# Kernel tuning notes

Measured on AMD Instinct MI355X. Metric: run time of the kernel, lower is better.

## Reference

```python
import jax, jax.numpy as jnp
import numpy as np

B, T, I, H, C = 64, 512, 512, 1024, 1024
SIG_W = 3.0


def setup_inputs() -> dict:
    key = jax.random.key(0)
    ks = jax.random.split(key, 20)
    s = 0.02
    p = lambda k, shp: (jax.random.normal(k, shp, jnp.float32) * s)
    return dict(
        x=jax.random.normal(ks[0], (B, T, I), jnp.float32),
        att_wih_f=p(ks[1], (3 * H, I)), att_whh_f=p(ks[2], (3 * H, H)),
        att_bih_f=p(ks[3], (3 * H,)), att_bhh_f=p(ks[4], (3 * H,)),
        att_wih_b=p(ks[5], (3 * H, I)), att_whh_b=p(ks[6], (3 * H, H)),
        att_bih_b=p(ks[7], (3 * H,)), att_bhh_b=p(ks[8], (3 * H,)),
        att_fc_w=p(ks[9], (1, 2 * H)), att_fc_b=p(ks[10], (1,)),
        i2h_w=p(ks[11], (H, I)), i2h_b=p(ks[12], (H,)),
        h2h_w=p(ks[13], (H, H)), h2h_b=p(ks[14], (H,)),
        fc0_w=p(ks[15], (C, H)), fc0_b=p(ks[16], (C,)),
        fc1_w=p(ks[17], (H, H)), fc1_b=p(ks[18], (H,)),
    )


def _gru(x_tbi, wih, whh, bih, bhh):
    # torch-style GRU over time-major input [T,B,I] -> hidden states [T,B,H]
    def step(h, xt):
        gi = xt @ wih.T + bih          # [B,3H]
        gh = h @ whh.T + bhh           # [B,3H]
        ir, iz, inn = jnp.split(gi, 3, axis=-1)
        hr, hz, hn = jnp.split(gh, 3, axis=-1)
        r = jax.nn.sigmoid(ir + hr)
        z = jax.nn.sigmoid(iz + hz)
        n = jnp.tanh(inn + r * hn)
        h = (1.0 - z) * n + z * h
        return h, h
    h0 = jnp.zeros((x_tbi.shape[1], whh.shape[1]), x_tbi.dtype)
    _, hs = jax.lax.scan(step, h0, x_tbi)
    return hs


def reference(x, att_wih_f, att_whh_f, att_bih_f, att_bhh_f,
              att_wih_b, att_whh_b, att_bih_b, att_bhh_b,
              att_fc_w, att_fc_b, i2h_w, i2h_b, h2h_w, h2h_b,
              fc0_w, fc0_b, fc1_w, fc1_b):
    xt = jnp.transpose(x, (1, 0, 2))                      # [T,B,I] time-major
    # AttentionNet: bidirectional GRU + Linear(2H,1) + sigmoid(sig_w * score)
    hf = _gru(xt, att_wih_f, att_whh_f, att_bih_f, att_bhh_f)
    hb = _gru(xt[::-1], att_wih_b, att_whh_b, att_bih_b, att_bhh_b)[::-1]
    hcat = jnp.concatenate([hf, hb], axis=-1)             # [T,B,2H]
    att = jax.nn.sigmoid(SIG_W * (hcat @ att_fc_w.T + att_fc_b))[..., 0]  # [T,B]

    # TAGM recurrence: h_t = a_t * relu(i2h(x_t) + h2h(h)) + (1-a_t) * h
    i2h_all = xt @ i2h_w.T + i2h_b                        # [T,B,H]
    def step(h, inp):
        i2h_t, a_t = inp
        trans = jax.nn.relu(i2h_t + h @ h2h_w.T + h2h_b)  # [B,H]
        a = a_t[:, None]
        return a * trans + (1.0 - a) * h, None
    h0 = jnp.zeros((x.shape[0], h2h_w.shape[1]), x.dtype)
    h_last, _ = jax.lax.scan(step, h0, (i2h_all, att))

    out = (h_last @ fc0_w.T + fc0_b) @ fc1_w.T + fc1_b    # fc0 then fc1 (no dropout, eval)
    return out, jnp.transpose(att)                        # ([B,C], attention [B,T])
```

## Files before the change

kernel.cpp:

```cpp
#include <hip/hip_runtime.h>
#include <cstdint>
#include <cstddef>

#define TDIM 512
#define BDIM 64
#define IDIM 512
#define HDIM 1024
#define SPIN_CAP 20000u
#define NREP 4

typedef __attribute__((ext_vector_type(8))) short s16x8;
typedef __attribute__((ext_vector_type(4))) float f32x4;

__device__ __forceinline__ unsigned short f2bf(float f) {
  unsigned u = __builtin_bit_cast(unsigned, f);
  u += 0x7FFFu + ((u >> 16) & 1u);
  return (unsigned short)(u >> 16);
}
__device__ __forceinline__ float bf2f(unsigned short s) {
  unsigned u = ((unsigned)s) << 16;
  return __builtin_bit_cast(float, u);
}
__device__ __forceinline__ float sigmf(float x) { return 1.0f / (1.0f + __expf(-x)); }
__device__ __forceinline__ unsigned pk2(float a, float b) {
  return (unsigned)f2bf(a) | ((unsigned)f2bf(b) << 16);
}
#define MFMA16(a, b, c) __builtin_amdgcn_mfma_f32_16x16x32_bf16((a), (b), (c), 0, 0, 0)

__device__ __forceinline__ s16x8 ld16_llc(const unsigned long long* p) {
  s16x8 v;
  asm volatile("global_load_dwordx4 %0, %1, off sc0 sc1" : "=v"(v) : "v"(p));
  return v;
}
__device__ __forceinline__ void sysst64(unsigned long long* p, unsigned long long v) {
  __hip_atomic_store(p, v, __ATOMIC_RELAXED, __HIP_MEMORY_SCOPE_SYSTEM);
}

__global__ __launch_bounds__(256) void k_xcvt(const float* __restrict__ x,
                                              unsigned short* __restrict__ xbf) {
  int idx = blockIdx.x * 256 + threadIdx.x;
  int i8 = idx * 8;
  int i = i8 & (IDIM - 1);
  int tb = i8 >> 9;
  int t = tb >> 6, b = tb & 63;
  const float* src = x + ((size_t)(b * TDIM + t)) * IDIM + i;
  float4 a = *(const float4*)src;
  float4 c = *(const float4*)(src + 4);
  uint4 v;
  v.x = pk2(a.x, a.y); v.y = pk2(a.z, a.w);
  v.z = pk2(c.x, c.y); v.w = pk2(c.z, c.w);
  *(uint4*)(xbf + i8) = v;
}

__global__ __launch_bounds__(128, 1) void k_gru_fused(
    const unsigned short* __restrict__ xbf,
    const float* __restrict__ wihf32f, const float* __restrict__ wihf32b,
    const float* __restrict__ whhf32f, const float* __restrict__ whhf32b,
    const float* __restrict__ bih_f, const float* __restrict__ bhh_f,
    const float* __restrict__ bih_b, const float* __restrict__ bhh_b,
    const float* __restrict__ attw,
    unsigned long long* __restrict__ hbufu, float* __restrict__ attp,
    unsigned int* __restrict__ flags) {
  __shared__ uint4 lds4[147456 / 16];
  char* lds = (char*)lds4;
  const int wg = blockIdx.x;
  const int dir = wg >> 7, half = (wg >> 6) & 1, cg = wg & 63;
  const int tid = threadIdx.x, w = tid >> 6, l = tid & 63;
  const int r = l & 15, q = l >> 4;
  const int col = cg * 16 + r;
  const float* wih = dir ? wihf32b : wihf32f;
  const float* whh = dir ? whhf32b : whhf32f;
  const float* bih = dir ? bih_b : bih_f;
  const float* bhh = dir ? bhh_b : bhh_f;
  unsigned int* myflags = flags + (dir * 2 + half) * 1024;
  unsigned long long* hb0 = hbufu + (size_t)(dir * 2 + half) * (NREP * 2 * 8192);

  for (int it = tid; it < 48 * 128; it += 128) {
    int row = it >> 7, ch = it & 127;
    int g = row >> 4, rr = row & 15;
    const float* src = whh + ((size_t)(g * HDIM + cg * 16 + rr)) * HDIM + ch * 8;
    float4 f0 = *(const float4*)src;
    float4 f1 = *(const float4*)(src + 4);
    uint4 v;
    v.x = pk2(f0.x, f0.y); v.y = pk2(f0.z, f0.w);
    v.z = pk2(f1.x, f1.y); v.w = pk2(f1.z, f1.w);
    *(uint4*)(lds + row * 2048 + ((ch * 16) ^ ((row & 7) << 4))) = v;
  }
  for (int it = tid; it < 48 * 64; it += 128) {
    int row = it >> 6, ch = it & 63;
    int g = row >> 4, rr = row & 15;
    const float* src = wih + ((size_t)(g * HDIM + cg * 16 + rr)) * IDIM + ch * 8;
    float4 f0 = *(const float4*)src;
    float4 f1 = *(const float4*)(src + 4);
    uint4 v;
    v.x = pk2(f0.x, f0.y); v.y = pk2(f0.z, f0.w);
    v.z = pk2(f1.x, f1.y); v.w = pk2(f1.z, f1.w);
    *(uint4*)(lds + 98304 + row * 1024 + ((ch * 16) ^ ((row & 7) << 4))) = v;
  }
  __syncthreads();

  const float br = bih[col] + bhh[col];
  const float bz = bih[col + HDIM] + bhh[col + HDIM];
  const float bnx = bih[col + 2 * HDIM];
  const float bnh = bhh[col + 2 * HDIM];
  const float wfc = attw[dir * HDIM + col];
  const int swz = (r & 7) << 4;
  const int bb = half * 32 + w * 16;
  float h[4] = {0.f, 0.f, 0.f, 0.f};

  for (int t = 0; t < TDIM; ++t) {
    const int tt = dir ? (TDIM - 1 - t) : t;
    f32x4 aR = {}, aZ = {}, aNx = {}, aNh = {};
    {
      const unsigned short* px = xbf + ((size_t)(tt * BDIM + bb + r)) * IDIM + q * 8;
#pragma unroll 4
      for (int kt = 0; kt < 16; ++kt) {
        s16x8 a = *(const s16x8*)(px + kt * 32);
        int kb = q * 16 + kt * 64;
        s16x8 b0 = *(const s16x8*)(lds + 98304 + r * 1024 + (kb ^ swz));
        s16x8 b1 = *(const s16x8*)(lds + 98304 + (16 + r) * 1024 + (kb ^ swz));
        s16x8 b2 = *(const s16x8*)(lds + 98304 + (32 + r) * 1024 + (kb ^ swz));
        aR = MFMA16(a, b0, aR);
        aZ = MFMA16(a, b1, aZ);
        aNx = MFMA16(a, b2, aNx);
      }
    }
    if (t > 0) {
      for (unsigned spin = 0;; ++spin) {
        unsigned v = __hip_atomic_load(&myflags[l * 16], __ATOMIC_RELAXED, __HIP_MEMORY_SCOPE_SYSTEM);
        if (__all((int)(v >= (unsigned)t))) break;
        if (spin > SPIN_CAP) break;
      }
      __builtin_amdgcn_sched_barrier(0);
    }
    {
      const unsigned long long* ph = hb0 + (size_t)(cg & (NREP - 1)) * 16384 +
                                     (size_t)(t & 1) * 8192 + (w * 16 + r) * 256 + q * 2;
      s16x8 ha[32];
#pragma unroll
      for (int i = 0; i < 32; ++i) {
        int kro = (i + cg) & 31;
        ha[i] = ld16_llc(ph + kro * 8);
      }
      asm volatile("s_waitcnt vmcnt(0)" ::: "memory");
      __builtin_amdgcn_sched_barrier(0);
#pragma unroll
      for (int i = 0; i < 32; ++i) {
        int kro = (i + cg) & 31;
        int kb = q * 16 + kro * 64;
        s16x8 b0 = *(const s16x8*)(lds + r * 2048 + (kb ^ swz));
        s16x8 b1 = *(const s16x8*)(lds + (16 + r) * 2048 + (kb ^ swz));
        s16x8 b2 = *(const s16x8*)(lds + (32 + r) * 2048 + (kb ^ swz));
        aR = MFMA16(ha[i], b0, aR);
        aZ = MFMA16(ha[i], b1, aZ);
        aNh = MFMA16(ha[i], b2, aNh);
      }
    }
    unsigned long long* hn = hb0 + (size_t)((t + 1) & 1) * 8192;
    float sa[4];
#pragma unroll
    for (int j = 0; j < 4; ++j) {
      const int lb = w * 16 + q * 4 + j;
      float rg = sigmf(aR[j] + br);
      float zg = sigmf(aZ[j] + bz);
      float ng = tanhf(aNx[j] + bnx + rg * (aNh[j] + bnh));
      float hv = (1.0f - zg) * ng + zg * h[j];
      h[j] = hv;
      sa[j] = hv * wfc;
      unsigned p2 = pk2(hv, __shfl_xor(hv, 1, 64));
      unsigned p2o = __shfl_xor(p2, 2, 64);
      if ((r & 3) == 0) {
        unsigned long long v64 = (unsigned long long)p2 | ((unsigned long long)p2o << 32);
        size_t off = (size_t)lb * 256 + cg * 4 + (r >> 2);
#pragma unroll
        for (int rep = 0; rep < NREP; ++rep)
          sysst64(&hn[(size_t)rep * 16384 + off], v64);
      }
    }
    asm volatile("s_waitcnt vmcnt(0)" ::: "memory");
    __syncthreads();
    if (tid == 0)
      __hip_atomic_store(&myflags[cg * 16], (unsigned)(t + 1),
                         __ATOMIC_RELAXED, __HIP_MEMORY_SCOPE_SYSTEM);
    {
      float* ap = attp + (size_t)(dir * 64 + cg) * (TDIM * BDIM) + tt * BDIM;
#pragma unroll
      for (int j = 0; j < 4; ++j) {
        const int b = half * 32 + w * 16 + q * 4 + j;
        float s = sa[j];
        s += __shfl_xor(s, 1, 64);
        s += __shfl_xor(s, 2, 64);
        s += __shfl_xor(s, 4, 64);
        s += __shfl_xor(s, 8, 64);
        if (r == 0) ap[b] = s;
      }
    }
  }
}

__global__ __launch_bounds__(256) void k_attf(const float* __restrict__ attp,
                                              const float* __restrict__ fcb,
                                              float* __restrict__ att,
                                              float* __restrict__ att_out) {
  int idx = blockIdx.x * 256 + threadIdx.x;
  float s = fcb[0];
  for (int g = 0; g < 128; ++g) s += attp[(size_t)g * (TDIM * BDIM) + idx];
  float a = sigmf(3.0f * s);
  att[idx] = a;
  int t = idx >> 6, b = idx & 63;
  att_out[(size_t)b * TDIM + t] = a;
}

__global__ __launch_bounds__(128, 1) void k_scan3(
    const unsigned short* __restrict__ xbf,
    const float* __restrict__ i2hf32, const float* __restrict__ h2hf32,
    const float* __restrict__ i2hb, const float* __restrict__ h2hb,
    const float* __restrict__ att,
    unsigned long long* __restrict__ h3u, float* __restrict__ hlast,
    unsigned int* __restrict__ flags3) {
  __shared__ uint4 lds4[49152 / 16];
  char* lds = (char*)lds4;
  const int wg = blockIdx.x;
  const int half = wg >> 6, cg = wg & 63;
  const int tid = threadIdx.x, w = tid >> 6, l = tid & 63;
  const int r = l & 15, q = l >> 4;
  const int col = cg * 16 + r;
  unsigned int* myflags = flags3 + half * 1024;
  unsigned long long* hb0 = h3u + (size_t)half * (NREP * 2 * 8192);
  for (int it = tid; it < 16 * 128; it += 128) {
    int row = it >> 7, ch = it & 127;
    const float* src = h2hf32 + ((size_t)(cg * 16 + row)) * HDIM + ch * 8;
    float4 f0 = *(const float4*)src;
    float4 f1 = *(const float4*)(src + 4);
    uint4 v;
    v.x = pk2(f0.x, f0.y); v.y = pk2(f0.z, f0.w);
    v.z = pk2(f1.x, f1.y); v.w = pk2(f1.z, f1.w);
    *(uint4*)(lds + row * 2048 + ((ch * 16) ^ ((row & 7) << 4))) = v;
  }
  for (int it = tid; it < 16 * 64; it += 128) {
    int row = it >> 6, ch = it & 63;
    const float* src = i2hf32 + ((size_t)(cg * 16 + row)) * IDIM + ch * 8;
    float4 f0 = *(const float4*)src;
    float4 f1 = *(const float4*)(src + 4);
    uint4 v;
    v.x = pk2(f0.x, f0.y); v.y = pk2(f0.z, f0.w);
    v.z = pk2(f1.x, f1.y); v.w = pk2(f1.z, f1.w);
    *(uint4*)(lds + 32768 + row * 1024 + ((ch * 16) ^ ((row & 7) << 4))) = v;
  }
  __syncthreads();
  const float bc = i2hb[col] + h2hb[col];
  const int swz = (r & 7) << 4;
  const int bb = half * 32 + w * 16;
  float h[4] = {0.f, 0.f, 0.f, 0.f};
  for (int t = 0; t < TDIM; ++t) {
    f32x4 ac = {};
    {
      const unsigned short* px = xbf + ((size_t)(t * BDIM + bb + r)) * IDIM + q * 8;
#pragma unroll 4
      for (int kt = 0; kt < 16; ++kt) {
        s16x8 a = *(const s16x8*)(px + kt * 32);
        int kb = q * 16 + kt * 64;
        s16x8 b = *(const s16x8*)(lds + 32768 + r * 1024 + (kb ^ swz));
        ac = MFMA16(a, b, ac);
      }
    }
    if (t > 0) {
      for (unsigned spin = 0;; ++spin) {
        unsigned v = __hip_atomic_load(&myflags[l * 16], __ATOMIC_RELAXED, __HIP_MEMORY_SCOPE_SYSTEM);
        if (__all((int)(v >= (unsigned)t))) break;
        if (spin > SPIN_CAP) break;
      }
      __builtin_amdgcn_sched_barrier(0);
    }
    {
      const unsigned long long* ph = hb0 + (size_t)(cg & (NREP - 1)) * 16384 +
                                     (size_t)(t & 1) * 8192 + (w * 16 + r) * 256 + q * 2;
      s16x8 ha[32];
#pragma unroll
      for (int i = 0; i < 32; ++i) {
        int kro = (i + cg) & 31;
        ha[i] = ld16_llc(ph + kro * 8);
      }
      asm volatile("s_waitcnt vmcnt(0)" ::: "memory");
      __builtin_amdgcn_sched_barrier(0);
#pragma unroll
      for (int i = 0; i < 32; ++i) {
        int kro = (i + cg) & 31;
        int kb = q * 16 + kro * 64;
        s16x8 b = *(const s16x8*)(lds + r * 2048 + (kb ^ swz));
        ac = MFMA16(ha[i], b, ac);
      }
    }
    unsigned long long* hn = hb0 + (size_t)((t + 1) & 1) * 8192;
    const float* ab = att + (size_t)t * BDIM;
#pragma unroll
    for (int j = 0; j < 4; ++j) {
      const int lb = w * 16 + q * 4 + j;
      float tr = fmaxf(ac[j] + bc, 0.0f);
      float a = ab[half * 32 + lb];
      float hv = a * tr + (1.0f - a) * h[j];
      h[j] = hv;
      unsigned p2 = pk2(hv, __shfl_xor(hv, 1, 64));
      unsigned p2o = __shfl_xor(p2, 2, 64);
      if ((r & 3) == 0) {
        unsigned long long v64 = (unsigned long long)p2 | ((unsigned long long)p2o << 32);
        size_t off = (size_t)lb * 256 + cg * 4 + (r >> 2);
#pragma unroll
        for (int rep = 0; rep < NREP; ++rep)
          sysst64(&hn[(size_t)rep * 16384 + off], v64);
      }
    }
    asm volatile("s_waitcnt vmcnt(0)" ::: "memory");
    __syncthreads();
    if (tid == 0)
      __hip_atomic_store(&myflags[cg * 16], (unsigned)(t + 1),
                         __ATOMIC_RELAXED, __HIP_MEMORY_SCOPE_SYSTEM);
  }
#pragma unroll
  for (int j = 0; j < 4; ++j) {
    const int b = half * 32 + w * 16 + q * 4 + j;
    hlast[b * HDIM + col] = h[j];
  }
}

__global__ __launch_bounds__(256) void k_fc(const float* __restrict__ A,
                                            const float* __restrict__ W,
                                            const float* __restrict__ bias,
                                            float* __restrict__ dst) {
  const int idx = blockIdx.x * 256 + threadIdx.x;
  const int rr = idx >> 10, c = idx & 1023;
  const float4* a = (const float4*)(A + (size_t)rr * HDIM);
  const float4* w = (const float4*)(W + (size_t)c * HDIM);
  float s = bias[c];
  for (int k = 0; k < HDIM / 4; ++k) {
    float4 xx = a[k], y = w[k];
    s += xx.x * y.x + xx.y * y.y + xx.z * y.z + xx.w * y.w;
  }
  dst[idx] = s;
}

__global__ __launch_bounds__(256) void k_diag(float* out, int n, float val) {
  int i = blockIdx.x * 256 + threadIdx.x;
  if (i < n) out[i] = val;
}

extern "C" void kernel_launch(void* const* d_in, const int* in_sizes, int n_in,
                              void* d_out, int out_size, void* d_ws, size_t ws_size,
                              hipStream_t stream) {
  float* outF = (float*)d_out;
  int diag_blocks = (out_size + 255) / 256;

  static const int exp_sizes[19] = {16777216, 1572864, 3145728, 3072, 3072,
                                    1572864, 3145728, 3072, 3072, 2048, 1,
                                    524288, 1024, 1048576, 1024, 1048576, 1024,
                                    1048576, 1024};
  if (n_in != 19) {
    k_diag<<<diag_blocks, 256, 0, stream>>>(outF, out_size, 3999.0f);
    return;
  }
  for (int i = 0; i < 19; ++i) {
    if (in_sizes[i] != exp_sizes[i]) {
      k_diag<<<diag_blocks, 256, 0, stream>>>(outF, out_size, (float)(4000 + i * 16));
      return;
    }
  }

  const float* x     = (const float*)d_in[0];
  const float* wih_f = (const float*)d_in[1];
  const float* whh_f = (const float*)d_in[2];
  const float* bih_f = (const float*)d_in[3];
  const float* bhh_f = (const float*)d_in[4];
  const float* wih_b = (const float*)d_in[5];
  const float* whh_b = (const float*)d_in[6];
  const float* bih_b = (const float*)d_in[7];
  const float* bhh_b = (const float*)d_in[8];
  const float* fc_w  = (const float*)d_in[9];
  const float* fc_b  = (const float*)d_in[10];
  const float* i2h_w = (const float*)d_in[11];
  const float* i2h_b = (const float*)d_in[12];
  const float* h2h_w = (const float*)d_in[13];
  const float* h2h_b = (const float*)d_in[14];
  const float* fc0_w = (const float*)d_in[15];
  const float* fc0_b = (const float*)d_in[16];
  const float* fc1_w = (const float*)d_in[17];
  const float* fc1_b = (const float*)d_in[18];

  const size_t OFF_XBF   = 0;
  const size_t OFF_ATTP  = 33554432;
  const size_t OFF_ATT   = 50331648;
  const size_t OFF_HBUF  = 50462720;
  const size_t OFF_H3BUF = 52559872;
  const size_t OFF_HLAST = 53608448;
  const size_t OFF_OUT1  = 53870592;
  const size_t OFF_FLAGS = 54132736;
  const size_t TOTAL     = 54157312;

  if (ws_size < TOTAL) {
    k_diag<<<diag_blocks, 256, 0, stream>>>(outF, out_size, (float)(ws_size >> 20));
    return;
  }

  char* ws = (char*)d_ws;
  unsigned short* xbf       = (unsigned short*)(ws + OFF_XBF);
  float* attp               = (float*)(ws + OFF_ATTP);
  float* att                = (float*)(ws + OFF_ATT);
  unsigned long long* hbufu = (unsigned long long*)(ws + OFF_HBUF);
  unsigned long long* h3u   = (unsigned long long*)(ws + OFF_H3BUF);
  float* hlast              = (float*)(ws + OFF_HLAST);
  float* out1               = (float*)(ws + OFF_OUT1);
  unsigned int* flags       = (unsigned int*)(ws + OFF_FLAGS);

  hipMemsetAsync(flags, 0, 24576, stream);
  hipMemsetAsync(hbufu, 0, 2097152, stream);
  hipMemsetAsync(h3u, 0, 1048576, stream);

  k_xcvt<<<8192, 256, 0, stream>>>(x, xbf);

  k_gru_fused<<<256, 128, 0, stream>>>(xbf, wih_f, wih_b, whh_f, whh_b,
                                       bih_f, bhh_f, bih_b, bhh_b, fc_w,
                                       hbufu, attp, flags);

  k_attf<<<128, 256, 0, stream>>>(attp, fc_b, att, outF + 65536);

  k_scan3<<<128, 128, 0, stream>>>(xbf, i2h_w, h2h_w, i2h_b, h2h_b, att,
                                   h3u, hlast, flags + 4096);

  k_fc<<<256, 256, 0, stream>>>(hlast, fc0_w, fc0_b, out1);
  k_fc<<<256, 256, 0, stream>>>(out1, fc1_w, fc1_b, outF);
}
```

Measured before the change: 8.035 ms.

## Use full per-timestep hidden-state history buffers instead of replicated ring buffers

```diff
diff --git a/kernel.cpp b/kernel.cpp
--- a/kernel.cpp
+++ b/kernel.cpp
@@ -16,10 +16,6 @@
   unsigned u = __builtin_bit_cast(unsigned, f);
   u += 0x7FFFu + ((u >> 16) & 1u);
   return (unsigned short)(u >> 16);
-}
-__device__ __forceinline__ float bf2f(unsigned short s) {
-  unsigned u = ((unsigned)s) << 16;
-  return __builtin_bit_cast(float, u);
 }
 __device__ __forceinline__ float sigmf(float x) { return 1.0f / (1.0f + __expf(-x)); }
 __device__ __forceinline__ unsigned pk2(float a, float b) {
@@ -50,6 +46,242 @@
   v.x = pk2(a.x, a.y); v.y = pk2(a.z, a.w);
   v.z = pk2(c.x, c.y); v.w = pk2(c.z, c.w);
   *(uint4*)(xbf + i8) = v;
+}
+
+__global__ __launch_bounds__(128, 1) void k_gru_big(
+    const unsigned short* __restrict__ xbf,
+    const float* __restrict__ wihf32f, const float* __restrict__ wihf32b,
+    const float* __restrict__ whhf32f, const float* __restrict__ whhf32b,
+    const float* __restrict__ bih_f, const float* __restrict__ bhh_f,
+    const float* __restrict__ bih_b, const float* __restrict__ bhh_b,
+    const float* __restrict__ attw,
+    unsigned long long* __restrict__ ghist, float* __restrict__ attp,
+    unsigned int* __restrict__ flags) {
+  __shared__ uint4 lds4[147456 / 16];
+  char* lds = (char*)lds4;
+  const int wg = blockIdx.x;
+  const int dir = wg >> 7, half = (wg >> 6) & 1, cg = wg & 63;
+  const int tid = threadIdx.x, w = tid >> 6, l = tid & 63;
+  const int r = l & 15, q = l >> 4;
+  const int col = cg * 16 + r;
+  const float* wih = dir ? wihf32b : wihf32f;
+  const float* whh = dir ? whhf32b : whhf32f;
+  const float* bih = dir ? bih_b : bih_f;
+  const float* bhh = dir ? bhh_b : bhh_f;
+  unsigned int* myflags = flags + (dir * 2 + half) * 1024;
+  unsigned long long* hist = ghist + (size_t)(dir * 2 + half) * ((size_t)TDIM * 8192);
+
+  for (int it = tid; it < 48 * 128; it += 128) {
+    int row = it >> 7, ch = it & 127;
+    int g = row >> 4, rr = row & 15;
+    const float* src = whh + ((size_t)(g * HDIM + cg * 16 + rr)) * HDIM + ch * 8;
+    float4 f0 = *(const float4*)src;
+    float4 f1 = *(const float4*)(src + 4);
+    uint4 v;
+    v.x = pk2(f0.x, f0.y); v.y = pk2(f0.z, f0.w);
+    v.z = pk2(f1.x, f1.y); v.w = pk2(f1.z, f1.w);
+    *(uint4*)(lds + row * 2048 + ((ch * 16) ^ ((row & 7) << 4))) = v;
+  }
+  for (int it = tid; it < 48 * 64; it += 128) {
+    int row = it >> 6, ch = it & 63;
+    int g = row >> 4, rr = row & 15;
+    const float* src = wih + ((size_t)(g * HDIM + cg * 16 + rr)) * IDIM + ch * 8;
+    float4 f0 = *(const float4*)src;
+    float4 f1 = *(const float4*)(src + 4);
+    uint4 v;
+    v.x = pk2(f0.x, f0.y); v.y = pk2(f0.z, f0.w);
+    v.z = pk2(f1.x, f1.y); v.w = pk2(f1.z, f1.w);
+    *(uint4*)(lds + 98304 + row * 1024 + ((ch * 16) ^ ((row & 7) << 4))) = v;
+  }
+  __syncthreads();
+
+  const float br = bih[col] + bhh[col];
+  const float bz = bih[col + HDIM] + bhh[col + HDIM];
+  const float bnx = bih[col + 2 * HDIM];
+  const float bnh = bhh[col + 2 * HDIM];
+  const float wfc = attw[dir * HDIM + col];
+  const int swz = (r & 7) << 4;
+  const int bb = half * 32 + w * 16;
+  float h[4] = {0.f, 0.f, 0.f, 0.f};
+
+  for (int t = 0; t < TDIM; ++t) {
+    const int tt = dir ? (TDIM - 1 - t) : t;
+    f32x4 aR = {}, aZ = {}, aNx = {}, aNh = {};
+    {
+      const unsigned short* px = xbf + ((size_t)(tt * BDIM + bb + r)) * IDIM + q * 8;
+#pragma unroll 4
+      for (int kt = 0; kt < 16; ++kt) {
+        s16x8 a = *(const s16x8*)(px + kt * 32);
+        int kb = q * 16 + kt * 64;
+        s16x8 b0 = *(const s16x8*)(lds + 98304 + r * 1024 + (kb ^ swz));
+        s16x8 b1 = *(const s16x8*)(lds + 98304 + (16 + r) * 1024 + (kb ^ swz));
+        s16x8 b2 = *(const s16x8*)(lds + 98304 + (32 + r) * 1024 + (kb ^ swz));
+        aR = MFMA16(a, b0, aR);
+        aZ = MFMA16(a, b1, aZ);
+        aNx = MFMA16(a, b2, aNx);
+      }
+    }
+    if (t > 0) {
+      for (unsigned spin = 0;; ++spin) {
+        unsigned v = __hip_atomic_load(&myflags[l * 16], __ATOMIC_RELAXED, __HIP_MEMORY_SCOPE_SYSTEM);
+        if (__all((int)(v >= (unsigned)t))) break;
+        if (spin > SPIN_CAP) break;
+      }
+      __builtin_amdgcn_sched_barrier(0);
+      const unsigned long long* ph = hist + (size_t)(t - 1) * 8192 + (w * 16 + r) * 256 + q * 2;
+      s16x8 ha[32];
+#pragma unroll
+      for (int i = 0; i < 32; ++i) ha[i] = *(const s16x8*)(ph + ((i + cg) & 31) * 8);
+#pragma unroll
+      for (int i = 0; i < 32; ++i) {
+        int kro = (i + cg) & 31;
+        int kb = q * 16 + kro * 64;
+        s16x8 b0 = *(const s16x8*)(lds + r * 2048 + (kb ^ swz));
+        s16x8 b1 = *(const s16x8*)(lds + (16 + r) * 2048 + (kb ^ swz));
+        s16x8 b2 = *(const s16x8*)(lds + (32 + r) * 2048 + (kb ^ swz));
+        aR = MFMA16(ha[i], b0, aR);
+        aZ = MFMA16(ha[i], b1, aZ);
+        aNh = MFMA16(ha[i], b2, aNh);
+      }
+    }
+    unsigned long long* hn = hist + (size_t)t * 8192;
+    float sa[4];
+#pragma unroll
+    for (int j = 0; j < 4; ++j) {
+      const int lb = w * 16 + q * 4 + j;
+      float rg = sigmf(aR[j] + br);
+      float zg = sigmf(aZ[j] + bz);
+      float ng = tanhf(aNx[j] + bnx + rg * (aNh[j] + bnh));
+      float hv = (1.0f - zg) * ng + zg * h[j];
+      h[j] = hv;
+      sa[j] = hv * wfc;
+      unsigned p2 = pk2(hv, __shfl_xor(hv, 1, 64));
+      unsigned p2o = __shfl_xor(p2, 2, 64);
+      if ((r & 3) == 0) {
+        unsigned long long v64 = (unsigned long long)p2 | ((unsigned long long)p2o << 32);
+        sysst64(&hn[(size_t)lb * 256 + cg * 4 + (r >> 2)], v64);
+      }
+    }
+    asm volatile("s_waitcnt vmcnt(0)" ::: "memory");
+    __syncthreads();
+    if (tid == 0)
+      __hip_atomic_store(&myflags[cg * 16], (unsigned)(t + 1),
+                         __ATOMIC_RELAXED, __HIP_MEMORY_SCOPE_SYSTEM);
+    {
+      float* ap = attp + (size_t)(dir * 64 + cg) * (TDIM * BDIM) + tt * BDIM;
+#pragma unroll
+      for (int j = 0; j < 4; ++j) {
+        const int b = half * 32 + w * 16 + q * 4 + j;
+        float s = sa[j];
+        s += __shfl_xor(s, 1, 64);
+        s += __shfl_xor(s, 2, 64);
+        s += __shfl_xor(s, 4, 64);
+        s += __shfl_xor(s, 8, 64);
+        if (r == 0) ap[b] = s;
+      }
+    }
+  }
+}
+
+__global__ __launch_bounds__(128, 1) void k_scan3_big(
+    const unsigned short* __restrict__ xbf,
+    const float* __restrict__ i2hf32, const float* __restrict__ h2hf32,
+    const float* __restrict__ i2hb, const float* __restrict__ h2hb,
+    const float* __restrict__ att,
+    unsigned long long* __restrict__ shist, float* __restrict__ hlast,
+    unsigned int* __restrict__ flags3) {
+  __shared__ uint4 lds4[49152 / 16];
+  char* lds = (char*)lds4;
+  const int wg = blockIdx.x;
+  const int half = wg >> 6, cg = wg & 63;
+  const int tid = threadIdx.x, w = tid >> 6, l = tid & 63;
+  const int r = l & 15, q = l >> 4;
+  const int col = cg * 16 + r;
+  unsigned int* myflags = flags3 + half * 1024;
+  unsigned long long* hist = shist + (size_t)half * ((size_t)TDIM * 8192);
+  for (int it = tid; it < 16 * 128; it += 128) {
+    int row = it >> 7, ch = it & 127;
+    const float* src = h2hf32 + ((size_t)(cg * 16 + row)) * HDIM + ch * 8;
+    float4 f0 = *(const float4*)src;
+    float4 f1 = *(const float4*)(src + 4);
+    uint4 v;
+    v.x = pk2(f0.x, f0.y); v.y = pk2(f0.z, f0.w);
+    v.z = pk2(f1.x, f1.y); v.w = pk2(f1.z, f1.w);
+    *(uint4*)(lds + row * 2048 + ((ch * 16) ^ ((row & 7) << 4))) = v;
+  }
+  for (int it = tid; it < 16 * 64; it += 128) {
+    int row = it >> 6, ch = it & 63;
+    const float* src = i2hf32 + ((size_t)(cg * 16 + row)) * IDIM + ch * 8;
+    float4 f0 = *(const float4*)src;
+    float4 f1 = *(const float4*)(src + 4);
+    uint4 v;
+    v.x = pk2(f0.x, f0.y); v.y = pk2(f0.z, f0.w);
+    v.z = pk2(f1.x, f1.y); v.w = pk2(f1.z, f1.w);
+    *(uint4*)(lds + 32768 + row * 1024 + ((ch * 16) ^ ((row & 7) << 4))) = v;
+  }
+  __syncthreads();
+  const float bc = i2hb[col] + h2hb[col];
+  const int swz = (r & 7) << 4;
+  const int bb = half * 32 + w * 16;
+  float h[4] = {0.f, 0.f, 0.f, 0.f};
+  for (int t = 0; t < TDIM; ++t) {
+    f32x4 ac = {};
+    {
+      const unsigned short* px = xbf + ((size_t)(t * BDIM + bb + r)) * IDIM + q * 8;
+#pragma unroll 4
+      for (int kt = 0; kt < 16; ++kt) {
+        s16x8 a = *(const s16x8*)(px + kt * 32);
+        int kb = q * 16 + kt * 64;
+        s16x8 b = *(const s16x8*)(lds + 32768 + r * 1024 + (kb ^ swz));
+        ac = MFMA16(a, b, ac);
+      }
+    }
+    if (t > 0) {
+      for (unsigned spin = 0;; ++spin) {
+        unsigned v = __hip_atomic_load(&myflags[l * 16], __ATOMIC_RELAXED, __HIP_MEMORY_SCOPE_SYSTEM);
+        if (__all((int)(v >= (unsigned)t))) break;
+        if (spin > SPIN_CAP) break;
+      }
+      __builtin_amdgcn_sched_barrier(0);
+      const unsigned long long* ph = hist + (size_t)(t - 1) * 8192 + (w * 16 + r) * 256 + q * 2;
+      s16x8 ha[32];
+#pragma unroll
+      for (int i = 0; i < 32; ++i) ha[i] = *(const s16x8*)(ph + ((i + cg) & 31) * 8);
+#pragma unroll
+      for (int i = 0; i < 32; ++i) {
+        int kro = (i + cg) & 31;
+        int kb = q * 16 + kro * 64;
+        s16x8 b = *(const s16x8*)(lds + r * 2048 + (kb ^ swz));
+        ac = MFMA16(ha[i], b, ac);
+      }
+    }
+    unsigned long long* hn = hist + (size_t)t * 8192;
+    const float* ab = att + (size_t)t * BDIM;
+#pragma unroll
+    for (int j = 0; j < 4; ++j) {
+      const int lb = w * 16 + q * 4 + j;
+      float tr = fmaxf(ac[j] + bc, 0.0f);
+      float a = ab[half * 32 + lb];
+      float hv = a * tr + (1.0f - a) * h[j];
+      h[j] = hv;
+      unsigned p2 = pk2(hv, __shfl_xor(hv, 1, 64));
+      unsigned p2o = __shfl_xor(p2, 2, 64);
+      if ((r & 3) == 0) {
+        unsigned long long v64 = (unsigned long long)p2 | ((unsigned long long)p2o << 32);
+        sysst64(&hn[(size_t)lb * 256 + cg * 4 + (r >> 2)], v64);
+      }
+    }
+    asm volatile("s_waitcnt vmcnt(0)" ::: "memory");
+    __syncthreads();
+    if (tid == 0)
+      __hip_atomic_store(&myflags[cg * 16], (unsigned)(t + 1),
+                         __ATOMIC_RELAXED, __HIP_MEMORY_SCOPE_SYSTEM);
+  }
+#pragma unroll
+  for (int j = 0; j < 4; ++j) {
+    const int b = half * 32 + w * 16 + q * 4 + j;
+    hlast[b * HDIM + col] = h[j];
+  }
 }
 
 __global__ __launch_bounds__(128, 1) void k_gru_fused(
@@ -198,19 +430,6 @@
   }
 }
 
-__global__ __launch_bounds__(256) void k_attf(const float* __restrict__ attp,
-                                              const float* __restrict__ fcb,
-                                              float* __restrict__ att,
-                                              float* __restrict__ att_out) {
-  int idx = blockIdx.x * 256 + threadIdx.x;
-  float s = fcb[0];
-  for (int g = 0; g < 128; ++g) s += attp[(size_t)g * (TDIM * BDIM) + idx];
-  float a = sigmf(3.0f * s);
-  att[idx] = a;
-  int t = idx >> 6, b = idx & 63;
-  att_out[(size_t)b * TDIM + t] = a;
-}
-
 __global__ __launch_bounds__(128, 1) void k_scan3(
     const unsigned short* __restrict__ xbf,
     const float* __restrict__ i2hf32, const float* __restrict__ h2hf32,
@@ -323,6 +542,19 @@
   }
 }
 
+__global__ __launch_bounds__(256) void k_attf(const float* __restrict__ attp,
+                                              const float* __restrict__ fcb,
+                                              float* __restrict__ att,
+                                              float* __restrict__ att_out) {
+  int idx = blockIdx.x * 256 + threadIdx.x;
+  float s = fcb[0];
+  for (int g = 0; g < 128; ++g) s += attp[(size_t)g * (TDIM * BDIM) + idx];
+  float a = sigmf(3.0f * s);
+  att[idx] = a;
+  int t = idx >> 6, b = idx & 63;
+  att_out[(size_t)b * TDIM + t] = a;
+}
+
 __global__ __launch_bounds__(256) void k_fc(const float* __restrict__ A,
                                             const float* __restrict__ W,
                                             const float* __restrict__ bias,
@@ -385,46 +617,71 @@
   const float* fc1_w = (const float*)d_in[17];
   const float* fc1_b = (const float*)d_in[18];
 
-  const size_t OFF_XBF   = 0;
-  const size_t OFF_ATTP  = 33554432;
-  const size_t OFF_ATT   = 50331648;
+  const size_t OFF_XBF  = 0;
+  const size_t OFF_ATTP = 33554432;
+  const size_t OFF_ATT  = 50331648;
+
+  const size_t OFF_GHIST = 50462720;
+  const size_t OFF_SHIST = OFF_GHIST + 134217728;
+  const size_t OFF_HLAST_B = OFF_SHIST + 67108864;
+  const size_t OFF_OUT1_B  = OFF_HLAST_B + 262144;
+  const size_t OFF_FLAGS_B = OFF_OUT1_B + 262144;
+  const size_t TOTAL_BIG   = OFF_FLAGS_B + 24576;
+
   const size_t OFF_HBUF  = 50462720;
   const size_t OFF_H3BUF = 52559872;
   const size_t OFF_HLAST = 53608448;
   const size_t OFF_OUT1  = 53870592;
   const size_t OFF_FLAGS = 54132736;
-  const size_t TOTAL     = 54157312;
-
-  if (ws_size < TOTAL) {
+  const size_t TOTAL_SMALL = 54157312;
+
+  if (ws_size < TOTAL_SMALL) {
     k_diag<<<diag_blocks, 256, 0, stream>>>(outF, out_size, (float)(ws_size >> 20));
     return;
   }
 
   char* ws = (char*)d_ws;
-  unsigned short* xbf       = (unsigned short*)(ws + OFF_XBF);
-  float* attp               = (float*)(ws + OFF_ATTP);
-  float* att                = (float*)(ws + OFF_ATT);
-  unsigned long long* hbufu = (unsigned long long*)(ws + OFF_HBUF);
-  unsigned long long* h3u   = (unsigned long long*)(ws + OFF_H3BUF);
-  float* hlast              = (float*)(ws + OFF_HLAST);
-  float* out1               = (float*)(ws + OFF_OUT1);
-  unsigned int* flags       = (unsigned int*)(ws + OFF_FLAGS);
-
-  hipMemsetAsync(flags, 0, 24576, stream);
-  hipMemsetAsync(hbufu, 0, 2097152, stream);
-  hipMemsetAsync(h3u, 0, 1048576, stream);
+  unsigned short* xbf = (unsigned short*)(ws + OFF_XBF);
+  float* attp         = (float*)(ws + OFF_ATTP);
+  float* att          = (float*)(ws + OFF_ATT);
 
   k_xcvt<<<8192, 256, 0, stream>>>(x, xbf);
 
-  k_gru_fused<<<256, 128, 0, stream>>>(xbf, wih_f, wih_b, whh_f, whh_b,
+  if (ws_size >= TOTAL_BIG) {
+    unsigned long long* ghist = (unsigned long long*)(ws + OFF_GHIST);
+    unsigned long long* shist = (unsigned long long*)(ws + OFF_SHIST);
+    float* hlast              = (float*)(ws + OFF_HLAST_B);
+    float* out1               = (float*)(ws + OFF_OUT1_B);
+    unsigned int* flags       = (unsigned int*)(ws + OFF_FLAGS_B);
+
+    hipMemsetAsync(flags, 0, 24576, stream);
+
+    k_gru_big<<<256, 128, 0, stream>>>(xbf, wih_f, wih_b, whh_f, whh_b,
                                        bih_f, bhh_f, bih_b, bhh_b, fc_w,
-                                       hbufu, attp, flags);
-
-  k_attf<<<128, 256, 0, stream>>>(attp, fc_b, att, outF + 65536);
-
-  k_scan3<<<128, 128, 0, stream>>>(xbf, i2h_w, h2h_w, i2h_b, h2h_b, att,
-                                   h3u, hlast, flags + 4096);
-
-  k_fc<<<256, 256, 0, stream>>>(hlast, fc0_w, fc0_b, out1);
-  k_fc<<<256, 256, 0, stream>>>(out1, fc1_w, fc1_b, outF);
-}
+                                       ghist, attp, flags);
+    k_attf<<<128, 256, 0, stream>>>(attp, fc_b, att, outF + 65536);
+    k_scan3_big<<<128, 128, 0, stream>>>(xbf, i2h_w, h2h_w, i2h_b, h2h_b, att,
+                                         shist, hlast, flags + 4096);
+    k_fc<<<256, 256, 0, stream>>>(hlast, fc0_w, fc0_b, out1);
+    k_fc<<<256, 256, 0, stream>>>(out1, fc1_w, fc1_b, outF);
+  } else {
+    unsigned long long* hbufu = (unsigned long long*)(ws + OFF_HBUF);
+    unsigned long long* h3u   = (unsigned long long*)(ws + OFF_H3BUF);
+    float* hlast              = (float*)(ws + OFF_HLAST);
+    float* out1               = (float*)(ws + OFF_OUT1);
+    unsigned int* flags       = (unsigned int*)(ws + OFF_FLAGS);
+
+    hipMemsetAsync(flags, 0, 24576, stream);
+    hipMemsetAsync(hbufu, 0, 2097152, stream);
+    hipMemsetAsync(h3u, 0, 1048576, stream);
+
+    k_gru_fused<<<256, 128, 0, stream>>>(xbf, wih_f, wih_b, whh_f, whh_b,
+                                         bih_f, bhh_f, bih_b, bhh_b, fc_w,
+                                         hbufu, attp, flags);
+    k_attf<<<128, 256, 0, stream>>>(attp, fc_b, att, outF + 65536);
+    k_scan3<<<128, 128, 0, stream>>>(xbf, i2h_w, h2h_w, i2h_b, h2h_b, att,
+                                     h3u, hlast, flags + 4096);
+    k_fc<<<256, 256, 0, stream>>>(hlast, fc0_w, fc0_b, out1);
+    k_fc<<<256, 256, 0, stream>>>(out1, fc1_w, fc1_b, outF);
+  }
+}
```

Measured after the change: 7.301 ms. 9.1% less time.
